# Kernel tuning notes

Measured on AMD Instinct MI355X. Metric: run time of the kernel, lower is better.

The kernel has to match this reference:

```python
import jax, jax.numpy as jnp
import numpy as np

B, S, E = 2, 2048, 1024
H = 16
D = E // H  # head_dim = 64


def setup_inputs() -> dict:
    key = jax.random.key(0)
    ks = jax.random.split(key, 11)
    s = 1.0 / np.sqrt(E)
    return {
        "x": jax.random.normal(ks[0], (B, S, E), dtype=jnp.float32),
        "Wq": jax.random.uniform(ks[1], (E, E), jnp.float32, -s, s),
        "bq": jnp.zeros((E,), jnp.float32),
        "Wk": jax.random.uniform(ks[2], (E, E), jnp.float32, -s, s),
        "bk": jnp.zeros((E,), jnp.float32),
        "Wv": jax.random.uniform(ks[3], (E, E), jnp.float32, -s, s),
        "bv": jnp.zeros((E,), jnp.float32),
        "Wo": jax.random.uniform(ks[4], (E, E), jnp.float32, -s, s),
        "bo": jnp.zeros((E,), jnp.float32),
        "J_attn": jax.random.normal(ks[5], (H, D, D), jnp.float32) * 0.02,
        "lambda_attn": jnp.float32(0.5),
    }


def reference(x, Wq, bq, Wk, bk, Wv, bv, Wo, bo, J_attn, lambda_attn):
    b, s, _ = x.shape
    scale = jnp.sqrt(jnp.float32(D))

    def split_heads(y):  # [b,s,E] -> [b,H,s,D]
        return y.reshape(b, s, H, D).transpose(0, 2, 1, 3)

    Q = split_heads(x @ Wq.T + bq)
    K = split_heads(x @ Wk.T + bk)
    V = split_heads(x @ Wv.T + bv)

    attn_scores = jnp.einsum('bhid,bhjd->bhij', Q, K) / scale

    Qn = jnp.tanh(Q)
    Kn = jnp.tanh(K)
    # fold J into Qn first (small [H,D,D] contraction), then one big matmul
    QJ = jnp.einsum('bhid,hde->bhie', Qn, J_attn)
    delta = jnp.einsum('bhie,bhje->bhij', QJ, Kn)

    attn_scores = attn_scores + lambda_attn * delta
    attn_probs = jax.nn.softmax(attn_scores, axis=-1)

    out = jnp.einsum('bhij,bhjd->bhid', attn_probs, V)
    out = out.transpose(0, 2, 1, 3).reshape(b, s, E)
    return out @ Wo.T + bo
```

## Files before the change

### kernel.cpp

```cpp
#include <hip/hip_runtime.h>
#include <math.h>

#define NH 16

typedef __bf16 bf16x8 __attribute__((ext_vector_type(8)));
typedef float f32x4 __attribute__((ext_vector_type(4)));

__device__ __forceinline__ unsigned short f2bf(float f) {
  unsigned u = __float_as_uint(f);
  u += 0x7fffu + ((u >> 16) & 1u);
  return (unsigned short)(u >> 16);
}
__device__ __forceinline__ float bf2f(unsigned short h) {
  return __uint_as_float(((unsigned)h) << 16);
}
__device__ __forceinline__ float fexp2(float x) {
  return __builtin_amdgcn_exp2f(x);
}
__device__ __forceinline__ float fast_tanh16(float x) {
  return 1.f - 2.f * __builtin_amdgcn_rcpf(fexp2(16.f * x) + 1.f);
}
__device__ __forceinline__ void gl_lds16(const void* g, void* l) {
  __builtin_amdgcn_global_load_lds((const __attribute__((address_space(1))) void*)g,
                                   (__attribute__((address_space(3))) void*)l, 16, 0, 0);
}
union Frag8 { bf16x8 v; unsigned short u[8]; };
union FragU { bf16x8 v; unsigned u[4]; };
union FragQ { bf16x8 v; unsigned long long q[2]; };

__global__ __launch_bounds__(256) void prep_all(const float* __restrict__ x,
                                                const float* __restrict__ Wq,
                                                const float* __restrict__ Wk,
                                                const float* __restrict__ Wv,
                                                const float* __restrict__ Wo,
                                                const float* __restrict__ J,
                                                const float* __restrict__ lam_p,
                                                unsigned short* __restrict__ xh,
                                                unsigned short* __restrict__ wcat3,
                                                unsigned short* __restrict__ wocat,
                                                unsigned short* __restrict__ Jt)
{
  __shared__ float T[64][65];
  const int bid = blockIdx.x, tid = threadIdx.x;
  if (bid >= 8192) {
    const int h = bid - 8192;
    const float lam = lam_p[0] * 1.44269504f;
#pragma unroll
    for (int c = 0; c < 4; ++c) {
      int i = tid + c*256;
      int d = i >> 4, e4 = i & 15;
      float4 v = *(const float4*)&J[(size_t)h*4096 + d*64 + e4*4];
      T[d][e4*4+0] = v.x; T[d][e4*4+1] = v.y; T[d][e4*4+2] = v.z; T[d][e4*4+3] = v.w;
    }
    __syncthreads();
    const int e = tid >> 2, d0 = (tid & 3) * 16;
#pragma unroll
    for (int j4 = 0; j4 < 4; ++j4) {
      ushort4 o;
      o.x = f2bf(lam * T[d0+j4*4+0][e]);
      o.y = f2bf(lam * T[d0+j4*4+1][e]);
      o.z = f2bf(lam * T[d0+j4*4+2][e]);
      o.w = f2bf(lam * T[d0+j4*4+3][e]);
      *(ushort4*)&Jt[((size_t)h*64 + e)*64 + d0 + j4*4] = o;
    }
    return;
  }
  if (bid < 4096) {
    int i = bid * 256 + tid;
    float4 v = *(const float4*)&x[(size_t)i*4];
    ushort4 o;
    o.x = f2bf(v.x); o.y = f2bf(v.y); o.z = f2bf(v.z); o.w = f2bf(v.w);
    *(ushort4*)&xh[(size_t)i*4] = o;
  } else if (bid < 7168) {
    int i = (bid - 4096) * 256 + tid;
    int sel = i >> 18, loc = i & 262143;
    const float* src = (sel == 0) ? Wq : (sel == 1) ? Wk : Wv;
    float4 v = *(const float4*)&src[(size_t)loc*4];
    ushort4 o;
    o.x = f2bf(v.x); o.y = f2bf(v.y); o.z = f2bf(v.z); o.w = f2bf(v.w);
    *(ushort4*)&wcat3[(size_t)i*4] = o;
  } else {
    int i = (bid - 7168) * 256 + tid;
    int r = i >> 8, c = i & 255;
    float4 v = *(const float4*)&Wo[(size_t)r*1024 + c*4];
    ushort4 hi, lo;
    hi.x = f2bf(v.x); lo.x = f2bf(v.x - bf2f(hi.x));
    hi.y = f2bf(v.y); lo.y = f2bf(v.y - bf2f(hi.y));
    hi.z = f2bf(v.z); lo.z = f2bf(v.z - bf2f(hi.z));
    hi.w = f2bf(v.w); lo.w = f2bf(v.w - bf2f(hi.w));
    *(ushort4*)&wocat[(size_t)r*2048 + c*4]        = hi;
    *(ushort4*)&wocat[(size_t)r*2048 + 1024 + c*4] = lo;
  }
}

__global__ __launch_bounds__(256) void gemm_qkv(const unsigned short* __restrict__ A,
                                                const unsigned short* __restrict__ W,
                                                const float* __restrict__ bq,
                                                const float* __restrict__ bk,
                                                const float* __restrict__ bv,
                                                unsigned short* __restrict__ Qcat,
                                                unsigned short* __restrict__ Kcat,
                                                unsigned short* __restrict__ Vt)
{
  __shared__ unsigned short S[32768];
  const int tid = threadIdx.x, lane = tid & 63, wq = tid >> 6;
  const int l15 = lane & 15, lq = lane >> 4;
  const int n0 = blockIdx.x * 128, m0 = blockIdx.y * 128;
  const int wr = (wq & 1) * 64, wc = (wq >> 1) * 64;
  const int mode = n0 >> 10;

  f32x4 acc[4][4];
#pragma unroll
  for (int mb = 0; mb < 4; ++mb)
#pragma unroll
    for (int nb = 0; nb < 4; ++nb) { f32x4 z = {0.f,0.f,0.f,0.f}; acc[mb][nb] = z; }

  const unsigned short* mat = (wq < 2) ? A : W;
  const int rbase = (wq < 2) ? m0 : n0;
  const int srow = lane >> 3, sslot = lane & 7;

  auto STAGE = [&](int buf, int k0) {
    unsigned short* lb = S + buf*16384 + (wq >> 1) * 8192;
#pragma unroll
    for (int t = 0; t < 8; ++t) {
      int row = (wq & 1) * 64 + t*8 + srow;
      int chunk = sslot ^ (row & 7);
      gl_lds16(mat + (size_t)(rbase + row)*1024 + k0 + chunk*8,
               lb + ((wq & 1) * 64 + t*8) * 64);
    }
  };

  int cur = 0;
  STAGE(0, 0);
  __syncthreads();

  for (int k0 = 0; k0 < 1024; k0 += 64) {
    if (k0 + 64 < 1024) STAGE(cur ^ 1, k0 + 64);
    const unsigned short* Sc = S + cur*16384;
#pragma unroll
    for (int kk = 0; kk < 2; ++kk) {
      int c = kk*4 + lq;
      bf16x8 af[4], bf_[4];
#pragma unroll
      for (int mb = 0; mb < 4; ++mb) {
        int m = wr + mb*16 + l15;
        af[mb] = *(const bf16x8*)&Sc[m*64 + (c ^ (m & 7))*8];
      }
#pragma unroll
      for (int nb = 0; nb < 4; ++nb) {
        int n = wc + nb*16 + l15;
        bf_[nb] = *(const bf16x8*)&Sc[8192 + n*64 + (c ^ (n & 7))*8];
      }
#pragma unroll
      for (int mb = 0; mb < 4; ++mb)
#pragma unroll
        for (int nb = 0; nb < 4; ++nb)
          acc[mb][nb] = __builtin_amdgcn_mfma_f32_16x16x32_bf16(af[mb], bf_[nb], acc[mb][nb], 0,0,0);
    }
    __syncthreads();
    cur ^= 1;
  }

  const float* bias = (mode == 0) ? bq : (mode == 1) ? bk : bv;
  float bvv[4];
#pragma unroll
  for (int nb = 0; nb < 4; ++nb) bvv[nb] = bias[((n0 & 1023) + wc + nb*16 + l15)];

  if (mode == 2) {
#pragma unroll
    for (int mb = 0; mb < 4; ++mb) {
      int mrow = m0 + wr + mb*16 + lq*4;
      int b = mrow >> 11, s0 = mrow & 2047;
#pragma unroll
      for (int nb = 0; nb < 4; ++nb) {
        int n = (n0 & 1023) + wc + nb*16 + l15;
        int h = n >> 6, d = n & 63;
        ushort4 o;
        o.x = f2bf(acc[mb][nb][0] + bvv[nb]);
        o.y = f2bf(acc[mb][nb][1] + bvv[nb]);
        o.z = f2bf(acc[mb][nb][2] + bvv[nb]);
        o.w = f2bf(acc[mb][nb][3] + bvv[nb]);
        *(ushort4*)&Vt[((size_t)(b*NH + h)*64 + d)*2048 + s0] = o;
      }
    }
    return;
  }

#pragma unroll
  for (int mb = 0; mb < 4; ++mb) {
#pragma unroll
    for (int r = 0; r < 4; ++r) {
      int m = m0 + wr + mb*16 + lq*4 + r;
      int b = m >> 11, s = m & 2047;
#pragma unroll
      for (int nb = 0; nb < 4; ++nb) {
        float v = acc[mb][nb][r] + bvv[nb];
        int n = (n0 & 1023) + wc + nb*16 + l15;
        int h = n >> 6, d = n & 63;
        size_t row = ((size_t)(b*NH + h)*2048 + s)*128;
        if (mode == 0) {
          Qcat[row + d] = f2bf(v * 0.18033688f);
        } else {
          Kcat[row + d]      = f2bf(v);
          Kcat[row + 64 + d] = f2bf(1.f - 2.f * __builtin_amdgcn_rcpf(__expf(2.f*v) + 1.f));
        }
      }
    }
  }
}

__global__ __launch_bounds__(256) void build_qj2(unsigned short* __restrict__ Qcat,
                                                 const unsigned short* __restrict__ Jt)
{
  const int tid = threadIdx.x, lane = tid & 63, wq = tid >> 6;
  const int l15 = lane & 15, lq = lane >> 4;
  const int bh = blockIdx.y, row0 = blockIdx.x * 128;
  const int h = bh & (NH-1);

  bf16x8 jf[4][2];
#pragma unroll
  for (int nb = 0; nb < 4; ++nb)
#pragma unroll
    for (int kst = 0; kst < 2; ++kst)
      jf[nb][kst] = *(const bf16x8*)&Jt[((size_t)h*64 + nb*16 + l15)*64 + kst*32 + lq*8];

  Frag8 af[2][2];
#pragma unroll
  for (int mb = 0; mb < 2; ++mb) {
    const unsigned short* qp = Qcat + ((size_t)(bh*2048 + row0 + wq*32 + mb*16 + l15))*128 + lq*8;
#pragma unroll
    for (int kst = 0; kst < 2; ++kst) {
      Frag8 raw;
      raw.v = *(const bf16x8*)(qp + kst*32);
#pragma unroll
      for (int j = 0; j < 8; ++j) {
        float t = fast_tanh16(bf2f(raw.u[j]));
        af[mb][kst].u[j] = (unsigned short)(__float_as_uint(t) >> 16);
      }
    }
  }

  f32x4 acc[2][4];
#pragma unroll
  for (int mb = 0; mb < 2; ++mb)
#pragma unroll
    for (int nb = 0; nb < 4; ++nb) { f32x4 z = {0.f,0.f,0.f,0.f}; acc[mb][nb] = z; }
#pragma unroll
  for (int kst = 0; kst < 2; ++kst)
#pragma unroll
    for (int mb = 0; mb < 2; ++mb)
#pragma unroll
      for (int nb = 0; nb < 4; ++nb)
        acc[mb][nb] = __builtin_amdgcn_mfma_f32_16x16x32_bf16(af[mb][kst].v, jf[nb][kst], acc[mb][nb], 0,0,0);

#pragma unroll
  for (int mb = 0; mb < 2; ++mb)
#pragma unroll
    for (int r = 0; r < 4; ++r) {
      size_t rowb = ((size_t)(bh*2048 + row0 + wq*32 + mb*16 + lq*4 + r))*128 + 64;
#pragma unroll
      for (int nb = 0; nb < 4; ++nb)
        Qcat[rowb + nb*16 + l15] = f2bf(acc[mb][nb][r]);
    }
}

__global__ __launch_bounds__(256, 4) void flash7(
    const unsigned short* __restrict__ Qcat, const unsigned short* __restrict__ Kcat,
    const unsigned short* __restrict__ Vt, float* __restrict__ OP0,
    float* __restrict__ OP1, float* __restrict__ OP2, float* __restrict__ lpart)
{
  __shared__ unsigned short Ks[64*128];
  __shared__ unsigned short Vs[64*64];
  const int tid = threadIdx.x, lane = tid & 63, wq = tid >> 6;
  const int l15 = lane & 15, lq = lane >> 4;
  const int bid = blockIdx.x;
  const int bh = (((bid >> 3) & 3) << 3) | (bid & 7);
  const int inner = bid >> 5;
  const int row0 = (inner & 15) * 128;
  const int ks = inner >> 4;
  const int jt0 = ks * 11;
  const int jtN = jt0 + ((ks < 2) ? 11 : 10);

  Frag8 qf[2][4];
#pragma unroll
  for (int nb = 0; nb < 2; ++nb) {
    const unsigned short* qp = Qcat + ((size_t)(bh*2048 + row0 + wq*32 + nb*16 + l15))*128 + lq*8;
#pragma unroll
    for (int kst = 0; kst < 4; ++kst)
      qf[nb][kst].v = *(const bf16x8*)(qp + kst*32);
  }

  FragU ones;
  ones.u[0] = 0x3F803F80u; ones.u[1] = 0x3F803F80u;
  ones.u[2] = 0x3F803F80u; ones.u[3] = 0x3F803F80u;

  f32x4 o[4][2];
  f32x4 lacc[2];
  { f32x4 z = {0.f,0.f,0.f,0.f}; lacc[0] = z; lacc[1] = z; }
#pragma unroll
  for (int db = 0; db < 4; ++db)
#pragma unroll
    for (int nb = 0; nb < 2; ++nb) { f32x4 z = {0.f,0.f,0.f,0.f}; o[db][nb] = z; }

  const unsigned short* kgb = Kcat + ((size_t)bh*2048)*128;
  const unsigned short* vg  = Vt + (size_t)bh*64*2048;

  for (int jt = jt0; jt < jtN; ++jt) {
    __syncthreads();
#pragma unroll
    for (int t = 0; t < 4; ++t) {
      int g = (wq*4 + t)*4 + (lane >> 4);
      int slot = lane & 15;
      int chunk = (slot & 8) | ((slot ^ g) & 7);
      gl_lds16(kgb + (size_t)(jt*64 + g)*128 + chunk*8, Ks + (wq*4 + t)*512);
    }
#pragma unroll
    for (int t = 0; t < 2; ++t) {
      int rv = (wq*2 + t)*8 + (lane >> 3);
      int chunk = (lane & 7) ^ (rv & 7);
      gl_lds16(vg + (size_t)rv*2048 + jt*64 + chunk*8, Vs + (wq*2 + t)*512);
    }
    __syncthreads();

#pragma unroll
    for (int t = 0; t < 2; ++t) {
      unsigned P2[2][2][2];
#pragma unroll
      for (int kk = 0; kk < 2; ++kk) {
        const int kb = 2*t + kk;
        bf16x8 af[4];
#pragma unroll
        for (int kst = 0; kst < 4; ++kst) {
          int key = kb*16 + l15;
          int c = kst*4 + lq;
          int slot = (c & 8) | ((c ^ key) & 7);
          af[kst] = *(const bf16x8*)&Ks[key*128 + slot*8];
        }
        f32x4 s[2];
        { f32x4 z = {0.f,0.f,0.f,0.f}; s[0] = z; s[1] = z; }
        __builtin_amdgcn_s_setprio(1);
#pragma unroll
        for (int kst = 0; kst < 4; ++kst) {
          s[0] = __builtin_amdgcn_mfma_f32_16x16x32_bf16(af[kst], qf[0][kst].v, s[0], 0,0,0);
          s[1] = __builtin_amdgcn_mfma_f32_16x16x32_bf16(af[kst], qf[1][kst].v, s[1], 0,0,0);
        }
        __builtin_amdgcn_s_setprio(0);
#pragma unroll
        for (int nb = 0; nb < 2; ++nb) {
          float e0 = fexp2(s[nb][0]), e1 = fexp2(s[nb][1]);
          float e2 = fexp2(s[nb][2]), e3 = fexp2(s[nb][3]);
          P2[nb][kk][0] = __builtin_amdgcn_perm(__float_as_uint(e1), __float_as_uint(e0), 0x07060302u);
          P2[nb][kk][1] = __builtin_amdgcn_perm(__float_as_uint(e3), __float_as_uint(e2), 0x07060302u);
        }
      }

      FragU bfr[2];
#pragma unroll
      for (int nb = 0; nb < 2; ++nb) {
        bfr[nb].u[0] = P2[nb][0][0];
        bfr[nb].u[1] = P2[nb][0][1];
        bfr[nb].u[2] = P2[nb][1][0];
        bfr[nb].u[3] = P2[nb][1][1];
      }
      __builtin_amdgcn_s_setprio(1);
      lacc[0] = __builtin_amdgcn_mfma_f32_16x16x32_bf16(ones.v, bfr[0].v, lacc[0], 0,0,0);
      lacc[1] = __builtin_amdgcn_mfma_f32_16x16x32_bf16(ones.v, bfr[1].v, lacc[1], 0,0,0);

      const int c0 = 4*t + (lq >> 1);
      const int woff = 4*(lq & 1);
#pragma unroll
      for (int db = 0; db < 4; ++db) {
        int d = db*16 + l15;
        FragQ va;
        va.q[0] = *(const unsigned long long*)&Vs[d*64 + ((c0     ^ (d & 7))*8) + woff];
        va.q[1] = *(const unsigned long long*)&Vs[d*64 + (((c0+2) ^ (d & 7))*8) + woff];
        o[db][0] = __builtin_amdgcn_mfma_f32_16x16x32_bf16(va.v, bfr[0].v, o[db][0], 0,0,0);
        o[db][1] = __builtin_amdgcn_mfma_f32_16x16x32_bf16(va.v, bfr[1].v, o[db][1], 0,0,0);
      }
      __builtin_amdgcn_s_setprio(0);
    }
  }

  float* OP = (ks == 0) ? OP0 : (ks == 1) ? OP1 : OP2;
#pragma unroll
  for (int nb = 0; nb < 2; ++nb) {
    int qrow = row0 + wq*32 + nb*16 + l15;
    if (lq == 0) lpart[(size_t)ks*65536 + bh*2048 + qrow] = lacc[nb][0];
#pragma unroll
    for (int db = 0; db < 4; ++db)
#pragma unroll
      for (int r = 0; r < 4; ++r) {
        int d = db*16 + lq*4 + r;
        OP[(size_t)(bh*64 + d)*2048 + qrow] = o[db][nb][r];
      }
  }
}

__global__ __launch_bounds__(256) void combine3(const float* __restrict__ OP0,
                                                const float* __restrict__ OP1,
                                                const float* __restrict__ OP2,
                                                const float* __restrict__ lpart,
                                                unsigned short* __restrict__ attcat)
{
  __shared__ float Ts[64*68];
  __shared__ float Ls[64];
  const int tid = threadIdx.x;
  const int bh = blockIdx.y, s0 = blockIdx.x * 64;
  const int b = bh >> 4, h = bh & (NH-1);
#pragma unroll
  for (int c = 0; c < 4; ++c) {
    int fid = tid + c*256;
    int d = fid >> 4, s4 = fid & 15;
    size_t gi = ((size_t)(bh*64 + d))*2048 + s0 + s4*4;
    float4 a = *(const float4*)&OP0[gi];
    float4 bb = *(const float4*)&OP1[gi];
    float4 cc = *(const float4*)&OP2[gi];
    Ts[(s4*4+0)*68 + d] = a.x + bb.x + cc.x;
    Ts[(s4*4+1)*68 + d] = a.y + bb.y + cc.y;
    Ts[(s4*4+2)*68 + d] = a.z + bb.z + cc.z;
    Ts[(s4*4+3)*68 + d] = a.w + bb.w + cc.w;
  }
  if (tid < 64) {
    size_t li = (size_t)bh*2048 + s0 + tid;
    Ls[tid] = lpart[li] + lpart[65536 + li] + lpart[131072 + li];
  }
  __syncthreads();
  const int sl = tid >> 2, d0 = (tid & 3) * 16;
  const float inv = 1.f / Ls[sl];
  const size_t rb = ((size_t)(b*2048 + s0 + sl))*2048 + h*64;
#pragma unroll
  for (int j4 = 0; j4 < 4; ++j4) {
    float4 t = *(const float4*)&Ts[sl*68 + d0 + j4*4];
    float v0 = t.x*inv, v1 = t.y*inv, v2 = t.z*inv, v3 = t.w*inv;
    ushort4 hi, lo;
    hi.x = f2bf(v0); lo.x = f2bf(v0 - bf2f(hi.x));
    hi.y = f2bf(v1); lo.y = f2bf(v1 - bf2f(hi.y));
    hi.z = f2bf(v2); lo.z = f2bf(v2 - bf2f(hi.z));
    hi.w = f2bf(v3); lo.w = f2bf(v3 - bf2f(hi.w));
    *(ushort4*)&attcat[rb + d0 + j4*4]        = hi;
    *(ushort4*)&attcat[rb + 1024 + d0 + j4*4] = lo;
  }
}

__global__ __launch_bounds__(512) void gemm3b(const unsigned short* __restrict__ A,
                                              const unsigned short* __restrict__ W,
                                              const float* __restrict__ bias,
                                              float* __restrict__ out)
{
  __shared__ unsigned short S[65536];
  const int tid = threadIdx.x, lane = tid & 63, wid = tid >> 6;
  const int l15 = lane & 15, lq = lane >> 4;
  const int n0 = blockIdx.x * 128, m0 = blockIdx.y * 128;
  const int wrow = wid >> 2, wcol = wid & 3;

  f32x4 acc[4][2];
#pragma unroll
  for (int mb = 0; mb < 4; ++mb)
#pragma unroll
    for (int nb = 0; nb < 2; ++nb) { f32x4 z = {0.f,0.f,0.f,0.f}; acc[mb][nb] = z; }

  const int region = wid >> 1;
  const unsigned short* mat = (region < 2) ? A : W;
  const int rbase = (region < 2) ? m0 : n0;
  const int koff  = (region & 1) * 1024;
  const int rhalf = (wid & 1) * 64;
  const int srow = lane >> 3, sslot = lane & 7;

  auto STAGE = [&](int buf, int k0) {
    unsigned short* lb = S + buf*32768 + region*8192 + rhalf*64;
#pragma unroll
    for (int t = 0; t < 8; ++t) {
      int row = rhalf + t*8 + srow;
      int chunk = sslot ^ (row & 7);
      gl_lds16(mat + (size_t)(rbase + row)*2048 + koff + k0 + chunk*8,
               lb + t*512);
    }
  };

  int cur = 0;
  STAGE(0, 0);
  __syncthreads();

  for (int k0 = 0; k0 < 1024; k0 += 64) {
    if (k0 + 64 < 1024) STAGE(cur ^ 1, k0 + 64);
    const unsigned short* Sc = S + cur*32768;
#pragma unroll
    for (int kk = 0; kk < 2; ++kk) {
      int c = kk*4 + lq;
      bf16x8 ah[4], al[4], bh_[2], bl_[2];
#pragma unroll
      for (int mb = 0; mb < 4; ++mb) {
        int m = wrow*64 + mb*16 + l15;
        int so = (c ^ (m & 7))*8;
        ah[mb] = *(const bf16x8*)&Sc[m*64 + so];
        al[mb] = *(const bf16x8*)&Sc[8192 + m*64 + so];
      }
#pragma unroll
      for (int nb = 0; nb < 2; ++nb) {
        int n = wcol*32 + nb*16 + l15;
        int so = (c ^ (n & 7))*8;
        bh_[nb] = *(const bf16x8*)&Sc[16384 + n*64 + so];
        bl_[nb] = *(const bf16x8*)&Sc[24576 + n*64 + so];
      }
#pragma unroll
      for (int mb = 0; mb < 4; ++mb)
#pragma unroll
        for (int nb = 0; nb < 2; ++nb) {
          acc[mb][nb] = __builtin_amdgcn_mfma_f32_16x16x32_bf16(ah[mb], bh_[nb], acc[mb][nb], 0,0,0);
          acc[mb][nb] = __builtin_amdgcn_mfma_f32_16x16x32_bf16(al[mb], bh_[nb], acc[mb][nb], 0,0,0);
          acc[mb][nb] = __builtin_amdgcn_mfma_f32_16x16x32_bf16(ah[mb], bl_[nb], acc[mb][nb], 0,0,0);
        }
    }
    __syncthreads();
    cur ^= 1;
  }

  float bvv[2];
#pragma unroll
  for (int nb = 0; nb < 2; ++nb) bvv[nb] = bias[n0 + wcol*32 + nb*16 + l15];
#pragma unroll
  for (int mb = 0; mb < 4; ++mb)
#pragma unroll
    for (int r = 0; r < 4; ++r) {
      int m = m0 + wrow*64 + mb*16 + lq*4 + r;
#pragma unroll
      for (int nb = 0; nb < 2; ++nb) {
        int n = n0 + wcol*32 + nb*16 + l15;
        out[(size_t)m*1024 + n] = acc[mb][nb][r] + bvv[nb];
      }
    }
}

extern "C" void kernel_launch(void* const* d_in, const int* in_sizes, int n_in,
                              void* d_out, int out_size, void* d_ws, size_t ws_size,
                              hipStream_t stream)
{
  const float* x   = (const float*)d_in[0];
  const float* Wq  = (const float*)d_in[1];
  const float* bq  = (const float*)d_in[2];
  const float* Wk  = (const float*)d_in[3];
  const float* bk  = (const float*)d_in[4];
  const float* Wv  = (const float*)d_in[5];
  const float* bv  = (const float*)d_in[6];
  const float* Wo  = (const float*)d_in[7];
  const float* bo  = (const float*)d_in[8];
  const float* J   = (const float*)d_in[9];
  const float* lam = (const float*)d_in[10];

  char* p = (char*)d_ws;
  char* regionA = p;
  unsigned short* xh     = (unsigned short*)p;  p += (size_t)4096*1024*2;
  unsigned short* wcat3  = (unsigned short*)p;  p += (size_t)3072*1024*2;
  unsigned short* Jt     = (unsigned short*)p;  p += (size_t)16*64*64*2;
  p += (size_t)2*1024*1024;
  unsigned short* Qcat   = (unsigned short*)p;  p += (size_t)65536*128*2;
  unsigned short* Kcat   = (unsigned short*)p;  p += (size_t)65536*128*2;
  unsigned short* Vt     = (unsigned short*)p;  p += (size_t)32*64*2048*2;
  unsigned short* wocat  = (unsigned short*)p;  p += (size_t)1024*2048*2;
  unsigned short* attcat = (unsigned short*)p;  p += (size_t)4096*2048*2;
  float*          OP0    = (float*)p;           p += (size_t)32*64*2048*4;
  float*          OP1    = (float*)p;           p += (size_t)32*64*2048*4;
  float*          lpart  = (float*)p;           p += (size_t)3*65536*4;
  float*          OP2    = (float*)regionA;
  float* out = (float*)d_out;

  dim3 blk(256);

  prep_all<<<dim3(8208), blk, 0, stream>>>(x, Wq, Wk, Wv, Wo, J, lam, xh, wcat3, wocat, Jt);
  gemm_qkv<<<dim3(24, 32), blk, 0, stream>>>(xh, wcat3, bq, bk, bv, Qcat, Kcat, Vt);
  build_qj2<<<dim3(16, 32), blk, 0, stream>>>(Qcat, Jt);
  flash7<<<dim3(1536), blk, 0, stream>>>(Qcat, Kcat, Vt, OP0, OP1, OP2, lpart);
  combine3<<<dim3(32, 32), blk, 0, stream>>>(OP0, OP1, OP2, lpart, attcat);
  gemm3b<<<dim3(8, 32), dim3(512), 0, stream>>>(attcat, wocat, bo, out);
}
```

Baseline: 231.9 us.

## Drop split-KV flash attention and fuse normalization/combine into flash epilogue

Each flash block now handles the full key range (32 tiles) instead of one of three KV splits. It normalizes its output in registers and writes the bf16 hi/lo attention output directly through an LDS transpose. This removes the combine kernel and the fp32 partial-output round trip through global memory. The grid shrinks from 1536 to 512 blocks, which may leave the GPU less occupied and make each block's serial loop longer.

```diff
diff --git a/kernel.cpp b/kernel.cpp
--- a/kernel.cpp
+++ b/kernel.cpp
@@ -264,22 +264,19 @@
     }
 }
 
-__global__ __launch_bounds__(256, 4) void flash7(
+__global__ __launch_bounds__(256, 4) void flash8(
     const unsigned short* __restrict__ Qcat, const unsigned short* __restrict__ Kcat,
-    const unsigned short* __restrict__ Vt, float* __restrict__ OP0,
-    float* __restrict__ OP1, float* __restrict__ OP2, float* __restrict__ lpart)
+    const unsigned short* __restrict__ Vt, unsigned short* __restrict__ attcat)
 {
-  __shared__ unsigned short Ks[64*128];
-  __shared__ unsigned short Vs[64*64];
+  __shared__ __align__(16) char smem[24576];
+  unsigned short* Ks = (unsigned short*)smem;
+  unsigned short* Vs = (unsigned short*)(smem + 16384);
   const int tid = threadIdx.x, lane = tid & 63, wq = tid >> 6;
   const int l15 = lane & 15, lq = lane >> 4;
   const int bid = blockIdx.x;
   const int bh = (((bid >> 3) & 3) << 3) | (bid & 7);
   const int inner = bid >> 5;
-  const int row0 = (inner & 15) * 128;
-  const int ks = inner >> 4;
-  const int jt0 = ks * 11;
-  const int jtN = jt0 + ((ks < 2) ? 11 : 10);
+  const int row0 = inner * 128;
 
   Frag8 qf[2][4];
 #pragma unroll
@@ -305,7 +302,7 @@
   const unsigned short* kgb = Kcat + ((size_t)bh*2048)*128;
   const unsigned short* vg  = Vt + (size_t)bh*64*2048;
 
-  for (int jt = jt0; jt < jtN; ++jt) {
+  for (int jt = 0; jt < 32; ++jt) {
     __syncthreads();
 #pragma unroll
     for (int t = 0; t < 4; ++t) {
@@ -381,64 +378,43 @@
     }
   }
 
-  float* OP = (ks == 0) ? OP0 : (ks == 1) ? OP1 : OP2;
-#pragma unroll
-  for (int nb = 0; nb < 2; ++nb) {
-    int qrow = row0 + wq*32 + nb*16 + l15;
-    if (lq == 0) lpart[(size_t)ks*65536 + bh*2048 + qrow] = lacc[nb][0];
-#pragma unroll
-    for (int db = 0; db < 4; ++db)
-#pragma unroll
-      for (int r = 0; r < 4; ++r) {
-        int d = db*16 + lq*4 + r;
-        OP[(size_t)(bh*64 + d)*2048 + qrow] = o[db][nb][r];
-      }
-  }
-}
-
-__global__ __launch_bounds__(256) void combine3(const float* __restrict__ OP0,
-                                                const float* __restrict__ OP1,
-                                                const float* __restrict__ OP2,
-                                                const float* __restrict__ lpart,
-                                                unsigned short* __restrict__ attcat)
-{
-  __shared__ float Ts[64*68];
-  __shared__ float Ls[64];
-  const int tid = threadIdx.x;
-  const int bh = blockIdx.y, s0 = blockIdx.x * 64;
   const int b = bh >> 4, h = bh & (NH-1);
-#pragma unroll
-  for (int c = 0; c < 4; ++c) {
-    int fid = tid + c*256;
-    int d = fid >> 4, s4 = fid & 15;
-    size_t gi = ((size_t)(bh*64 + d))*2048 + s0 + s4*4;
-    float4 a = *(const float4*)&OP0[gi];
-    float4 bb = *(const float4*)&OP1[gi];
-    float4 cc = *(const float4*)&OP2[gi];
-    Ts[(s4*4+0)*68 + d] = a.x + bb.x + cc.x;
-    Ts[(s4*4+1)*68 + d] = a.y + bb.y + cc.y;
-    Ts[(s4*4+2)*68 + d] = a.z + bb.z + cc.z;
-    Ts[(s4*4+3)*68 + d] = a.w + bb.w + cc.w;
-  }
-  if (tid < 64) {
-    size_t li = (size_t)bh*2048 + s0 + tid;
-    Ls[tid] = lpart[li] + lpart[65536 + li] + lpart[131072 + li];
-  }
-  __syncthreads();
-  const int sl = tid >> 2, d0 = (tid & 3) * 16;
-  const float inv = 1.f / Ls[sl];
-  const size_t rb = ((size_t)(b*2048 + s0 + sl))*2048 + h*64;
-#pragma unroll
-  for (int j4 = 0; j4 < 4; ++j4) {
-    float4 t = *(const float4*)&Ts[sl*68 + d0 + j4*4];
-    float v0 = t.x*inv, v1 = t.y*inv, v2 = t.z*inv, v3 = t.w*inv;
-    ushort4 hi, lo;
-    hi.x = f2bf(v0); lo.x = f2bf(v0 - bf2f(hi.x));
-    hi.y = f2bf(v1); lo.y = f2bf(v1 - bf2f(hi.y));
-    hi.z = f2bf(v2); lo.z = f2bf(v2 - bf2f(hi.z));
-    hi.w = f2bf(v3); lo.w = f2bf(v3 - bf2f(hi.w));
-    *(ushort4*)&attcat[rb + d0 + j4*4]        = hi;
-    *(ushort4*)&attcat[rb + 1024 + d0 + j4*4] = lo;
+  const float inv0 = 1.f / lacc[0][0];
+  const float inv1 = 1.f / lacc[1][0];
+  float* Ts = (float*)smem;
+#pragma unroll
+  for (int half = 0; half < 2; ++half) {
+    __syncthreads();
+    if ((wq >> 1) == half) {
+#pragma unroll
+      for (int nb = 0; nb < 2; ++nb) {
+        const float inv = nb ? inv1 : inv0;
+        const int rl = (wq & 1)*32 + nb*16 + l15;
+#pragma unroll
+        for (int db = 0; db < 4; ++db)
+#pragma unroll
+          for (int r = 0; r < 4; ++r)
+            Ts[rl*65 + db*16 + lq*4 + r] = o[db][nb][r] * inv;
+      }
+    }
+    __syncthreads();
+    const int sl = tid >> 2, d0 = (tid & 3) * 16;
+    const int srow = row0 + half*64 + sl;
+    const size_t rb = ((size_t)(b*2048 + srow))*2048 + h*64;
+#pragma unroll
+    for (int j4 = 0; j4 < 4; ++j4) {
+      float v0 = Ts[sl*65 + d0 + j4*4 + 0];
+      float v1 = Ts[sl*65 + d0 + j4*4 + 1];
+      float v2 = Ts[sl*65 + d0 + j4*4 + 2];
+      float v3 = Ts[sl*65 + d0 + j4*4 + 3];
+      ushort4 hi, lo;
+      hi.x = f2bf(v0); lo.x = f2bf(v0 - bf2f(hi.x));
+      hi.y = f2bf(v1); lo.y = f2bf(v1 - bf2f(hi.y));
+      hi.z = f2bf(v2); lo.z = f2bf(v2 - bf2f(hi.z));
+      hi.w = f2bf(v3); lo.w = f2bf(v3 - bf2f(hi.w));
+      *(ushort4*)&attcat[rb + d0 + j4*4]        = hi;
+      *(ushort4*)&attcat[rb + 1024 + d0 + j4*4] = lo;
+    }
   }
 }
 
@@ -548,7 +524,6 @@
   const float* lam = (const float*)d_in[10];
 
   char* p = (char*)d_ws;
-  char* regionA = p;
   unsigned short* xh     = (unsigned short*)p;  p += (size_t)4096*1024*2;
   unsigned short* wcat3  = (unsigned short*)p;  p += (size_t)3072*1024*2;
   unsigned short* Jt     = (unsigned short*)p;  p += (size_t)16*64*64*2;
@@ -558,10 +533,6 @@
   unsigned short* Vt     = (unsigned short*)p;  p += (size_t)32*64*2048*2;
   unsigned short* wocat  = (unsigned short*)p;  p += (size_t)1024*2048*2;
   unsigned short* attcat = (unsigned short*)p;  p += (size_t)4096*2048*2;
-  float*          OP0    = (float*)p;           p += (size_t)32*64*2048*4;
-  float*          OP1    = (float*)p;           p += (size_t)32*64*2048*4;
-  float*          lpart  = (float*)p;           p += (size_t)3*65536*4;
-  float*          OP2    = (float*)regionA;
   float* out = (float*)d_out;
 
   dim3 blk(256);
@@ -569,7 +540,6 @@
   prep_all<<<dim3(8208), blk, 0, stream>>>(x, Wq, Wk, Wv, Wo, J, lam, xh, wcat3, wocat, Jt);
   gemm_qkv<<<dim3(24, 32), blk, 0, stream>>>(xh, wcat3, bq, bk, bv, Qcat, Kcat, Vt);
   build_qj2<<<dim3(16, 32), blk, 0, stream>>>(Qcat, Jt);
-  flash7<<<dim3(1536), blk, 0, stream>>>(Qcat, Kcat, Vt, OP0, OP1, OP2, lpart);
-  combine3<<<dim3(32, 32), blk, 0, stream>>>(OP0, OP1, OP2, lpart, attcat);
+  flash8<<<dim3(512), blk, 0, stream>>>(Qcat, Kcat, Vt, attcat);
   gemm3b<<<dim3(8, 32), dim3(512), 0, stream>>>(attcat, wocat, bo, out);
 }
```

Result: faster. 225.0 us (-3.0%).
